# Performance work log

Hardware: AMD Instinct MI355X
Metric: run time of the kernel (lower is better)

## Reference

```python
import jax, jax.numpy as jnp
import numpy as np

B, S, D = 1, 1024, 64
_EPS = 1e-15
_BND = 1.0 - 1e-7  # artanh domain clamp (mirrors geoopt projection)


def _sq(x):
    return jnp.sum(x * x, axis=-1, keepdims=True)


def _nrm(x):
    return jnp.sqrt(_sq(x) + _EPS)


def _normalize(x, axis, eps):
    n = jnp.sqrt(jnp.sum(x * x, axis=axis, keepdims=True))
    return x / jnp.maximum(n, eps)


def _mobius_add(x, y):
    x2, y2 = _sq(x), _sq(y)
    xy = jnp.sum(x * y, axis=-1, keepdims=True)
    num = (1.0 + 2.0 * xy + y2) * x + (1.0 - x2) * y
    den = 1.0 + 2.0 * xy + x2 * y2
    return num / jnp.maximum(den, _EPS)


def _expmap0(u):
    n = _nrm(u)
    return jnp.tanh(n) * u / n


def _logmap0(y):
    n = _nrm(y)
    return jnp.arctanh(jnp.clip(n, 0.0, _BND)) * y / n


def _dist(x, y):
    n = _nrm(_mobius_add(-x, y))[..., 0]
    return 2.0 * jnp.arctanh(jnp.clip(n, 0.0, _BND))


def _logmap(x, y):
    d = _mobius_add(-x, y)
    n = _nrm(d)
    lam = 2.0 / jnp.maximum(1.0 - _sq(x), _EPS)
    return (2.0 / lam) * jnp.arctanh(jnp.clip(n, 0.0, _BND)) * d / n


def _transp0back(x, v):
    return v / jnp.maximum(1.0 - _sq(x), _EPS)


def _forward(q_in, k_in, v_in, Wq, bq, Wk, bk, Wv, bv, Wo, bo,
             tau, gamma, tangent_scale, gumbel_u, v_rand_init):
    q = q_in @ Wq.T + bq
    k = k_in @ Wk.T + bk
    v = v_in @ Wv.T + bv

    q_hyp = _expmap0(q)   # [B,S,D]
    k_hyp = _expmap0(k)

    # all-pairs geodesic distances [B,S,S]
    dist = _dist(q_hyp[:, :, None, :], k_hyp[:, None, :, :])
    min_d = jnp.min(dist, axis=-1, keepdims=True)
    w_un = jnp.exp(-(dist - min_d))                         # unnormalized weights
    w_sum = jnp.sum(w_un, axis=-1, keepdims=True) + 1e-8
    w_probs = w_un / w_sum
    h = jnp.einsum('bqk,bkd->bqd', w_probs, v)

    # Einstein midpoint: weighted Euclidean centroid of pre-map keys -> manifold
    centroid_euc = jnp.einsum('bqk,bkd->bqd', w_un / w_sum, k)
    centroid_hyp = _expmap0(centroid_euc)                   # [B,S,D]

    c2k = _dist(centroid_hyp[:, :, None, :], k_hyp[:, None, :, :])  # [B,S,S]
    wnv = w_un / w_sum
    entropy = -jnp.sum(wnv * jnp.log(wnv + 1e-8), axis=-1, keepdims=True)
    eff_mass = jnp.exp(entropy)
    variance = jnp.sum(wnv * c2k ** 2, axis=-1, keepdims=True)
    tension = variance - tau * eff_mass                     # [B,S,1]

    # matrix-free TPCA power iteration on weighted local tangents
    k_local = _logmap(centroid_hyp[:, :, None, :], k_hyp[:, None, :, :])  # [B,S,S,D]
    weighted_k = k_local * jnp.sqrt(w_un[..., None] + 1e-8)
    v_r = _normalize(v_rand_init, axis=2, eps=1e-12)        # [B,S,D,1]
    for _ in range(3):
        proj = jnp.einsum('bqkd,bqdo->bqko', weighted_k, v_r)
        v_r = jnp.einsum('bqkd,bqko->bqdo', weighted_k, proj)
        v_r = _normalize(v_r, axis=2, eps=1e-12)
    w_proj_local = v_r[..., 0]                              # [B,S,D]
    w_proj_global = _transp0back(centroid_hyp, w_proj_local)

    q_tan = _logmap0(q_hyp)
    c_tan = _logmap0(centroid_hyp)
    fallback = _normalize(q_tan - c_tan, axis=-1, eps=1e-8)
    w_proj = jnp.where(variance > 1e-5, w_proj_global, fallback)

    h_norm = _nrm(h)
    h_comp = jnp.arcsinh(h_norm) * (h / (h_norm + 1e-8))

    # Pitchfork bifurcation (c = 1)
    x = jnp.sum(h_comp * w_proj, axis=-1, keepdims=True)
    diss = (tension > 0).astype(h.dtype)
    h_mag = _nrm(h_comp)
    amplitude = h_mag * jnp.tanh(tension) * diss
    g = -jnp.log(-jnp.log(gumbel_u))                        # gumbel noise, logits = 0
    y_soft = jax.nn.softmax(g / 0.5, axis=-1)
    y_hard = jax.nn.one_hot(jnp.argmax(y_soft, axis=-1), 2, dtype=h.dtype)
    gp = y_soft + jax.lax.stop_gradient(y_hard - y_soft)    # straight-through
    eps_g = (gp[..., 0] - gp[..., 1])[..., None]            # gp @ [1,-1]
    x_star = eps_g * amplitude
    delta_c = jnp.tanh(x_star - x)
    h_prime = h_comp + delta_c * w_proj
    hp_norm = _nrm(h_prime) + 1e-8
    h_pb = h_prime * (jnp.tanh(hp_norm * tangent_scale) / hp_norm)
    h_prime_hyp = _expmap0(h_pb)

    h_out_bif = _logmap0(h_prime_hyp)
    gate = jax.nn.sigmoid(gamma)
    h_fused = (1.0 - gate) * h + gate * h_out_bif
    return h_fused @ Wo.T + bo


def setup_inputs() -> dict:
    key = jax.random.key(0)
    ks = jax.random.split(key, 10)
    std = 0.02
    return {
        'q_in': jax.random.normal(ks[0], (B, S, D), jnp.float32),
        'k_in': jax.random.normal(ks[1], (B, S, D), jnp.float32),
        'v_in': jax.random.normal(ks[2], (B, S, D), jnp.float32),
        'Wq': std * jax.random.normal(ks[3], (D, D), jnp.float32),
        'bq': jnp.zeros((D,), jnp.float32),
        'Wk': std * jax.random.normal(ks[4], (D, D), jnp.float32),
        'bk': jnp.zeros((D,), jnp.float32),
        'Wv': std * jax.random.normal(ks[5], (D, D), jnp.float32),
        'bv': jnp.zeros((D,), jnp.float32),
        'Wo': std * jax.random.normal(ks[6], (D, D), jnp.float32),
        'bo': jnp.zeros((D,), jnp.float32),
        'tau': jnp.float32(5.0),
        'gamma': jnp.float32(0.0),
        'tangent_scale': jnp.float32(0.1),
        'gumbel_u': jax.random.uniform(ks[7], (B, S, 2), jnp.float32, 1e-6, 1.0 - 1e-6),
        'v_rand_init': jax.random.normal(ks[8], (B, S, D, 1), jnp.float32),
    }


def reference(q_in, k_in, v_in, Wq, bq, Wk, bk, Wv, bv, Wo, bo,
              tau, gamma, tangent_scale, gumbel_u, v_rand_init):
    return _forward(q_in, k_in, v_in, Wq, bq, Wk, bk, Wv, bv, Wo, bo,
                    tau, gamma, tangent_scale, gumbel_u, v_rand_init)
```

## Files before the change

### kernel.cpp

```cpp
#include <hip/hip_runtime.h>
#include <math.h>

#define S 1024
#define D 64
#define BND 0.99999994f
#define FINF 3.4e38f
#define C4(v,c) ((&(v).x)[c])

__device__ __forceinline__ float waveSum(float v){
  #pragma unroll
  for(int o=32;o>0;o>>=1) v += __shfl_xor(v,o,64);
  return v;
}
__device__ __forceinline__ float waveMin(float v){
  #pragma unroll
  for(int o=32;o>0;o>>=1) v = fminf(v,__shfl_xor(v,o,64));
  return v;
}
__device__ __forceinline__ float blockSum512(float v, float* red){
  float w = waveSum(v);
  int wid = threadIdx.x>>6;
  __syncthreads();
  if((threadIdx.x&63)==0) red[wid]=w;
  __syncthreads();
  float s=0.f;
  #pragma unroll
  for(int k=0;k<8;k++) s+=red[k];
  return s;
}
__device__ __forceinline__ float blockMin512(float v, float* red){
  float w = waveMin(v);
  int wid = threadIdx.x>>6;
  __syncthreads();
  if((threadIdx.x&63)==0) red[wid]=w;
  __syncthreads();
  float s=red[0];
  #pragma unroll
  for(int k=1;k<8;k++) s=fminf(s,red[k]);
  return s;
}
__device__ __forceinline__ float4 mk4(const float* a){
  float4 r; r.x=a[0]; r.y=a[1]; r.z=a[2]; r.w=a[3]; return r;
}

__global__ __launch_bounds__(64) void k_proj(
  const float* __restrict__ qin, const float* __restrict__ kin, const float* __restrict__ vin,
  const float* __restrict__ Wq, const float* __restrict__ bq,
  const float* __restrict__ Wk, const float* __restrict__ bk,
  const float* __restrict__ Wv, const float* __restrict__ bv,
  const float* __restrict__ vrand,
  float* __restrict__ q_hyp, float* __restrict__ k_hyp, float* __restrict__ kT,
  float* __restrict__ vproj, float* __restrict__ kproj,
  float* __restrict__ q2, float* __restrict__ k2, float* __restrict__ v_r)
{
  const int i = blockIdx.x, d = threadIdx.x;
  __shared__ __align__(16) float lq[D], lk[D], lv[D];
  lq[d]=qin[i*D+d]; lk[d]=kin[i*D+d]; lv[d]=vin[i*D+d];
  __syncthreads();
  float aq=bq[d], ak=bk[d], av=bv[d];
  const float4* wq4=(const float4*)(Wq + d*D);
  const float4* wk4=(const float4*)(Wk + d*D);
  const float4* wv4=(const float4*)(Wv + d*D);
  #pragma unroll
  for(int e=0;e<16;e++){
    float4 a=wq4[e], b=wk4[e], c=wv4[e];
    aq += lq[4*e]*a.x + lq[4*e+1]*a.y + lq[4*e+2]*a.z + lq[4*e+3]*a.w;
    ak += lk[4*e]*b.x + lk[4*e+1]*b.y + lk[4*e+2]*b.z + lk[4*e+3]*b.w;
    av += lv[4*e]*c.x + lv[4*e+1]*c.y + lv[4*e+2]*c.z + lv[4*e+3]*c.w;
  }
  float nq = sqrtf(waveSum(aq*aq)+1e-15f);
  float qh = tanhf(nq)*aq/nq;
  q_hyp[i*D+d]=qh;
  float q2v = waveSum(qh*qh);
  if(d==0) q2[i]=q2v;
  float nk = sqrtf(waveSum(ak*ak)+1e-15f);
  float kh = tanhf(nk)*ak/nk;
  k_hyp[i*D+d]=kh;
  kT[(size_t)d*S + i]=kh;
  float k2v = waveSum(kh*kh);
  if(d==0) k2[i]=k2v;
  vproj[i*D+d]=av;
  kproj[i*D+d]=ak;
  float vr = vrand[i*D+d];
  float nn = sqrtf(waveSum(vr*vr));
  v_r[i*D+d] = vr/fmaxf(nn,1e-12f);
}

__global__ __launch_bounds__(512,4) void k_wc(
  const float* __restrict__ q_hyp, const float* __restrict__ kT,
  const float* __restrict__ q2a, const float* __restrict__ k2a,
  const float* __restrict__ vproj, const float* __restrict__ kproj,
  float* __restrict__ wbuf, float* __restrict__ wsum, float* __restrict__ effm,
  float* __restrict__ h, float* __restrict__ c_hyp, float* __restrict__ c2)
{
  const int i0=blockIdx.x*2, tid=threadIdx.x;
  __shared__ __align__(16) float qv[2][D];
  __shared__ __align__(16) float wl[2][S];
  __shared__ __align__(16) float4 sA[1024];
  __shared__ __align__(16) float4 sB[1024];
  __shared__ float red[8];
  if(tid<128) qv[tid>>6][tid&63]=q_hyp[i0*D+tid];
  __syncthreads();
  const float x20=q2a[i0], x21=q2a[i0+1];
  const float B0=1.f-x20, B1=1.f-x21;
  const int jf=tid&255, dh=tid>>8;
  const float4* kT4=(const float4*)kT;
  {
    float4 p0={0,0,0,0}, p1={0,0,0,0};
    #pragma unroll 8
    for(int dd=0; dd<32; ++dd){
      const int d=(dh<<5)+dd;
      const float4 y=kT4[d*256+jf];
      const float c0=qv[0][d], c1=qv[1][d];
      p0.x+=c0*y.x; p0.y+=c0*y.y; p0.z+=c0*y.z; p0.w+=c0*y.w;
      p1.x+=c1*y.x; p1.y+=c1*y.y; p1.z+=c1*y.z; p1.w+=c1*y.w;
    }
    sA[(dh*2+0)*256+jf]=p0;
    sA[(dh*2+1)*256+jf]=p1;
  }
  __syncthreads();
  float dist[2][4];
  float mn0=FINF, mn1=FINF;
  if(tid<256){
    const float4 qa=sA[jf], qb=sA[512+jf];
    const float4 ra=sA[256+jf], rb=sA[768+jf];
    const float4 y2v=((const float4*)k2a)[jf];
    #pragma unroll
    for(int c=0;c<4;c++){
      const float y2=C4(y2v,c);
      {
        const float dot=C4(qa,c)+C4(qb,c);
        const float A=1.f-2.f*dot+y2;
        const float den=fmaxf(1.f-2.f*dot+x20*y2,1e-15f);
        const float num2=fmaxf(A*A*x20 + B0*B0*y2 - 2.f*A*B0*dot, 0.f);
        const float nn=sqrtf(num2/(den*den)+1e-15f);
        dist[0][c]=2.f*atanhf(fminf(nn,BND));
        mn0=fminf(mn0,dist[0][c]);
      }
      {
        const float dot=C4(ra,c)+C4(rb,c);
        const float A=1.f-2.f*dot+y2;
        const float den=fmaxf(1.f-2.f*dot+x21*y2,1e-15f);
        const float num2=fmaxf(A*A*x21 + B1*B1*y2 - 2.f*A*B1*dot, 0.f);
        const float nn=sqrtf(num2/(den*den)+1e-15f);
        dist[1][c]=2.f*atanhf(fminf(nn,BND));
        mn1=fminf(mn1,dist[1][c]);
      }
    }
  }
  const float m0=blockMin512(mn0,red);
  const float m1=blockMin512(mn1,red);
  float s0=0.f, s1=0.f;
  float w0c[4], w1c[4];
  if(tid<256){
    #pragma unroll
    for(int c=0;c<4;c++){
      w0c[c]=expf(m0-dist[0][c]); s0+=w0c[c];
      w1c[c]=expf(m1-dist[1][c]); s1+=w1c[c];
    }
    ((float4*)&wl[0][0])[jf]=mk4(w0c);
    ((float4*)&wl[1][0])[jf]=mk4(w1c);
    ((float4*)(wbuf+(size_t)i0*S))[jf]=mk4(w0c);
    ((float4*)(wbuf+(size_t)(i0+1)*S))[jf]=mk4(w1c);
  }
  s0=blockSum512(s0,red)+1e-8f;
  s1=blockSum512(s1,red)+1e-8f;
  if(tid==0){ wsum[i0]=s0; wsum[i0+1]=s1; }
  const float inv0=1.f/s0, inv1=1.f/s1;
  float e0=0.f, e1=0.f;
  if(tid<256){
    #pragma unroll
    for(int c=0;c<4;c++){
      const float p0=w0c[c]*inv0; e0 -= p0*logf(p0+1e-8f);
      const float p1=w1c[c]*inv1; e1 -= p1*logf(p1+1e-8f);
    }
  }
  e0=blockSum512(e0,red);
  e1=blockSum512(e1,red);
  if(tid==0){ effm[i0]=expf(e0); effm[i0+1]=expf(e1); }
  const int dq=tid&15, g=tid>>4;
  float4 ah0={0,0,0,0}, ah1={0,0,0,0}, ac0={0,0,0,0}, ac1={0,0,0,0};
  #pragma unroll 4
  for(int jj=0;jj<32;jj++){
    const int j=jj*32+g;
    const float4 yv=((const float4*)(vproj + j*D))[dq];
    const float4 yk=((const float4*)(kproj + j*D))[dq];
    const float u0=wl[0][j], u1=wl[1][j];
    ah0.x+=u0*yv.x; ah0.y+=u0*yv.y; ah0.z+=u0*yv.z; ah0.w+=u0*yv.w;
    ah1.x+=u1*yv.x; ah1.y+=u1*yv.y; ah1.z+=u1*yv.z; ah1.w+=u1*yv.w;
    ac0.x+=u0*yk.x; ac0.y+=u0*yk.y; ac0.z+=u0*yk.z; ac0.w+=u0*yk.w;
    ac1.x+=u1*yk.x; ac1.y+=u1*yk.y; ac1.z+=u1*yk.z; ac1.w+=u1*yk.w;
  }
  float* pA=(float*)sA;
  float* pB=(float*)sB;
  *(float4*)&pA[(g*2+0)*64+dq*4]=ah0;
  *(float4*)&pA[(g*2+1)*64+dq*4]=ah1;
  *(float4*)&pB[(g*2+0)*64+dq*4]=ac0;
  *(float4*)&pB[(g*2+1)*64+dq*4]=ac1;
  __syncthreads();
  if(tid<128){
    const int q=tid>>6, d=tid&63;
    float hs=0.f, cs=0.f;
    #pragma unroll 8
    for(int gg=0;gg<32;gg++){ hs+=pA[(gg*2+q)*64+d]; cs+=pB[(gg*2+q)*64+d]; }
    const float invq = q ? inv1 : inv0;
    h[(i0+q)*D+d]=hs*invq;
    const float ca=cs*invq;
    const float n=sqrtf(waveSum(ca*ca)+1e-15f);
    const float ch=tanhf(n)*ca/n;
    c_hyp[(i0+q)*D+d]=ch;
    const float c2v=waveSum(ch*ch);
    if(d==0) c2[i0+q]=c2v;
  }
}

__global__ __launch_bounds__(512,4) void k_pmega(
  const float* __restrict__ c_hyp, const float* __restrict__ k_hyp,
  const float* __restrict__ kT,
  const float* __restrict__ c2a, const float* __restrict__ k2a,
  const float* __restrict__ wbuf, const float* __restrict__ wsum,
  const float* __restrict__ effm, const float* __restrict__ tau_p,
  const float* __restrict__ h, const float* __restrict__ q_hyp,
  const float* __restrict__ q2a, const float* __restrict__ v_r,
  const float* __restrict__ gu, const float* __restrict__ gamma_p,
  const float* __restrict__ ts_p, const float* __restrict__ Wo,
  const float* __restrict__ bo, float* __restrict__ out)
{
  const int i0=blockIdx.x*2, tid=threadIdx.x;
  __shared__ __align__(16) float cv[2][D];
  __shared__ __align__(16) float vv[2][D];
  __shared__ __align__(16) float aal[2][S];
  __shared__ __align__(16) float bbl[2][S];
  __shared__ __align__(16) float prow[2][S];
  __shared__ __align__(16) float4 sA[1024];
  __shared__ __align__(16) float fus[2][D];
  __shared__ float red[8];
  __shared__ float scal[2][4];

  if(tid<128){ cv[tid>>6][tid&63]=c_hyp[i0*D+tid]; vv[tid>>6][tid&63]=v_r[i0*D+tid]; }
  __syncthreads();
  const float x20=c2a[i0], x21=c2a[i0+1];
  const float Bc0=1.f-x20, Bc1=1.f-x21;
  const float mB0=fmaxf(Bc0,1e-15f), mB1=fmaxf(Bc1,1e-15f);
  const float inv0=1.f/wsum[i0], inv1=1.f/wsum[i0+1];
  const int jf=tid&255, dh=tid>>8;
  const float4* kT4=(const float4*)kT;

  {
    float4 p0={0,0,0,0}, p1={0,0,0,0};
    #pragma unroll 8
    for(int dd=0; dd<32; ++dd){
      const int d=(dh<<5)+dd;
      const float4 y=kT4[d*256+jf];
      const float c0=cv[0][d], c1=cv[1][d];
      p0.x+=c0*y.x; p0.y+=c0*y.y; p0.z+=c0*y.z; p0.w+=c0*y.w;
      p1.x+=c1*y.x; p1.y+=c1*y.y; p1.z+=c1*y.z; p1.w+=c1*y.w;
    }
    sA[(dh*2+0)*256+jf]=p0;
    sA[(dh*2+1)*256+jf]=p1;
  }
  __syncthreads();
  float var0p=0.f, var1p=0.f;
  if(tid<256){
    const float4 qa=sA[jf], qb=sA[512+jf];
    const float4 ra=sA[256+jf], rb=sA[768+jf];
    const float4 y2v=((const float4*)k2a)[jf];
    const float4 w0v=((const float4*)(wbuf+(size_t)i0*S))[jf];
    const float4 w1v=((const float4*)(wbuf+(size_t)(i0+1)*S))[jf];
    float a0c[4],b0c[4],a1c[4],b1c[4];
    #pragma unroll
    for(int c=0;c<4;c++){
      const float y2=C4(y2v,c);
      {
        const float dot=C4(qa,c)+C4(qb,c);
        const float A=1.f-2.f*dot+y2;
        const float den=fmaxf(1.f-2.f*dot+x20*y2,1e-15f);
        const float num2=fmaxf(A*A*x20+Bc0*Bc0*y2-2.f*A*Bc0*dot,0.f);
        const float nn=sqrtf(num2/(den*den)+1e-15f);
        const float art=atanhf(fminf(nn,BND));
        const float w=C4(w0v,c);
        var0p += w*inv0*4.f*art*art;
        const float coef=sqrtf(w+1e-8f)*mB0*art/(nn*den);
        a0c[c]=-coef*A; b0c[c]=coef*Bc0;
      }
      {
        const float dot=C4(ra,c)+C4(rb,c);
        const float A=1.f-2.f*dot+y2;
        const float den=fmaxf(1.f-2.f*dot+x21*y2,1e-15f);
        const float num2=fmaxf(A*A*x21+Bc1*Bc1*y2-2.f*A*Bc1*dot,0.f);
        const float nn=sqrtf(num2/(den*den)+1e-15f);
        const float art=atanhf(fminf(nn,BND));
        const float w=C4(w1v,c);
        var1p += w*inv1*4.f*art*art;
        const float coef=sqrtf(w+1e-8f)*mB1*art/(nn*den);
        a1c[c]=-coef*A; b1c[c]=coef*Bc1;
      }
    }
    ((float4*)&aal[0][0])[jf]=mk4(a0c);
    ((float4*)&aal[1][0])[jf]=mk4(a1c);
    ((float4*)&bbl[0][0])[jf]=mk4(b0c);
    ((float4*)&bbl[1][0])[jf]=mk4(b1c);
  }
  const float var0=blockSum512(var0p,red);
  const float var1=blockSum512(var1p,red);
  if(tid==0){
    scal[0][0]=var0; scal[0][1]=var0 - tau_p[0]*effm[i0];
    scal[1][0]=var1; scal[1][1]=var1 - tau_p[0]*effm[i0+1];
  }

  const int dq=tid&15, g=tid>>4;
  for(int it=0; it<3; ++it){
    __syncthreads();
    if(tid<128){
      const int q=tid>>6, d=tid&63;
      const float cd=waveSum(cv[q][d]*vv[q][d]);
      if(d==0) scal[q][2]=cd;
    }
    __syncthreads();
    const float cdot0=scal[0][2], cdot1=scal[1][2];
    {
      float4 p0={0,0,0,0}, p1={0,0,0,0};
      #pragma unroll 8
      for(int dd=0; dd<32; ++dd){
        const int d=(dh<<5)+dd;
        const float4 y=kT4[d*256+jf];
        const float c0=vv[0][d], c1=vv[1][d];
        p0.x+=c0*y.x; p0.y+=c0*y.y; p0.z+=c0*y.z; p0.w+=c0*y.w;
        p1.x+=c1*y.x; p1.y+=c1*y.y; p1.z+=c1*y.z; p1.w+=c1*y.w;
      }
      sA[(dh*2+0)*256+jf]=p0;
      sA[(dh*2+1)*256+jf]=p1;
    }
    __syncthreads();
    float sal0p=0.f, sal1p=0.f;
    if(tid<256){
      const float4 qa=sA[jf], qb=sA[512+jf];
      const float4 ra=sA[256+jf], rb=sA[768+jf];
      const float4 av0=((float4*)&aal[0][0])[jf];
      const float4 av1=((float4*)&aal[1][0])[jf];
      const float4 bv0=((float4*)&bbl[0][0])[jf];
      const float4 bv1=((float4*)&bbl[1][0])[jf];
      float pr0[4], pr1[4];
      #pragma unroll
      for(int c=0;c<4;c++){
        const float t0=C4(qa,c)+C4(qb,c);
        const float t1=C4(ra,c)+C4(rb,c);
        const float p0=C4(av0,c)*cdot0 + C4(bv0,c)*t0;
        const float p1=C4(av1,c)*cdot1 + C4(bv1,c)*t1;
        pr0[c]=p0*C4(bv0,c); sal0p += p0*C4(av0,c);
        pr1[c]=p1*C4(bv1,c); sal1p += p1*C4(av1,c);
      }
      ((float4*)&prow[0][0])[jf]=mk4(pr0);
      ((float4*)&prow[1][0])[jf]=mk4(pr1);
    }
    const float sal0=blockSum512(sal0p,red);
    const float sal1=blockSum512(sal1p,red);
    float4 a0={0,0,0,0}, a1={0,0,0,0};
    #pragma unroll 4
    for(int jj=0;jj<32;jj++){
      const int j=jj*32+g;
      const float4 y=((const float4*)(k_hyp + j*D))[dq];
      const float u0=prow[0][j], u1=prow[1][j];
      a0.x+=u0*y.x; a0.y+=u0*y.y; a0.z+=u0*y.z; a0.w+=u0*y.w;
      a1.x+=u1*y.x; a1.y+=u1*y.y; a1.z+=u1*y.z; a1.w+=u1*y.w;
    }
    float* pA=(float*)sA;
    *(float4*)&pA[(g*2+0)*64+dq*4]=a0;
    *(float4*)&pA[(g*2+1)*64+dq*4]=a1;
    __syncthreads();
    if(tid<128){
      const int q=tid>>6, d=tid&63;
      float od=(q?sal1:sal0)*cv[q][d];
      #pragma unroll 8
      for(int gg=0;gg<32;gg++) od += pA[(gg*2+q)*64+d];
      const float nn=sqrtf(waveSum(od*od));
      vv[q][d]=od/fmaxf(nn,1e-12f);
    }
  }
  __syncthreads();

  if(tid<128){
    const int q=tid>>6, d=tid&63;
    const int i=i0+q;
    const float x2q = q ? x21 : x20;
    const float vd=vv[q][d];
    const float vars=scal[q][0], tns=scal[q][1];
    const float hd=h[i*D+d];
    const float qd=q_hyp[i*D+d];
    const float q2=q2a[i];
    const float wpg=vd/fmaxf(1.f-x2q,1e-15f);
    const float nq=sqrtf(q2+1e-15f);
    const float qt=atanhf(fminf(nq,BND))*qd/nq;
    const float ncn=sqrtf(x2q+1e-15f);
    const float ct=atanhf(fminf(ncn,BND))*cv[q][d]/ncn;
    const float df=qt-ct;
    const float nd=sqrtf(waveSum(df*df));
    const float fb=df/fmaxf(nd,1e-8f);
    const float wp=(vars>1e-5f)?wpg:fb;
    const float hn=sqrtf(waveSum(hd*hd)+1e-15f);
    const float hc=asinhf(hn)*hd/(hn+1e-8f);
    const float x=waveSum(hc*wp);
    const float hmag=sqrtf(waveSum(hc*hc)+1e-15f);
    const float amp=(tns>0.f)? hmag*tanhf(tns) : 0.f;
    const float u0=gu[i*2], u1=gu[i*2+1];
    const float eg=(u0>=u1)?1.f:-1.f;
    const float dc=tanhf(eg*amp - x);
    const float hp=hc+dc*wp;
    const float hpn=sqrtf(waveSum(hp*hp)+1e-15f)+1e-8f;
    const float hpb=hp*(tanhf(hpn*ts_p[0])/hpn);
    const float n2=sqrtf(waveSum(hpb*hpb)+1e-15f);
    const float hyp=tanhf(n2)*hpb/n2;
    const float n3=sqrtf(waveSum(hyp*hyp)+1e-15f);
    const float bif=atanhf(fminf(n3,BND))*hyp/n3;
    const float gate=1.f/(1.f+expf(-gamma_p[0]));
    fus[q][d]=(1.f-gate)*hd + gate*bif;
  }
  __syncthreads();
  if(tid<128){
    const int q=tid>>6, d=tid&63;
    float acc=bo[d];
    const float4* wo4=(const float4*)(Wo + d*D);
    #pragma unroll
    for(int e=0;e<16;e++){
      float4 wv=wo4[e];
      acc += fus[q][4*e]*wv.x + fus[q][4*e+1]*wv.y + fus[q][4*e+2]*wv.z + fus[q][4*e+3]*wv.w;
    }
    out[(i0+q)*D+d]=acc;
  }
}

extern "C" void kernel_launch(void* const* d_in, const int* in_sizes, int n_in,
                              void* d_out, int out_size, void* d_ws, size_t ws_size,
                              hipStream_t stream)
{
  const float* qin=(const float*)d_in[0];
  const float* kin=(const float*)d_in[1];
  const float* vin=(const float*)d_in[2];
  const float* Wq=(const float*)d_in[3];
  const float* bq=(const float*)d_in[4];
  const float* Wk=(const float*)d_in[5];
  const float* bk=(const float*)d_in[6];
  const float* Wv=(const float*)d_in[7];
  const float* bv=(const float*)d_in[8];
  const float* Wo=(const float*)d_in[9];
  const float* bo=(const float*)d_in[10];
  const float* tau=(const float*)d_in[11];
  const float* gamma=(const float*)d_in[12];
  const float* tscale=(const float*)d_in[13];
  const float* gu=(const float*)d_in[14];
  const float* vrand=(const float*)d_in[15];
  float* out=(float*)d_out;

  float* p=(float*)d_ws;
  float* q_hyp=p; p+=S*D;
  float* k_hyp=p; p+=S*D;
  float* kT=p;    p+=S*D;
  float* vproj=p; p+=S*D;
  float* kproj=p; p+=S*D;
  float* v_r=p;   p+=S*D;
  float* h=p;     p+=S*D;
  float* c_hyp=p; p+=S*D;
  float* q2=p;   p+=S;
  float* k2=p;   p+=S;
  float* c2=p;   p+=S;
  float* wsum=p; p+=S;
  float* effm=p; p+=S;
  float* wbuf=p; p+=(size_t)S*S;

  k_proj<<<S,64,0,stream>>>(qin,kin,vin,Wq,bq,Wk,bk,Wv,bv,vrand,
                            q_hyp,k_hyp,kT,vproj,kproj,q2,k2,v_r);
  k_wc<<<S/2,512,0,stream>>>(q_hyp,kT,q2,k2,vproj,kproj,
                             wbuf,wsum,effm,h,c_hyp,c2);
  k_pmega<<<S/2,512,0,stream>>>(c_hyp,k_hyp,kT,c2,k2,wbuf,wsum,effm,tau,
                                h,q_hyp,q2,v_r,gu,gamma,tscale,Wo,bo,out);
}
```

Baseline: 79.04 us.

## Fuse weight/centroid and power-iteration kernels, process four queries per block

Merges k_wc and k_pmega into a single kernel, so the 1024x1024 weight matrix and the h, c_hyp, wsum and effm intermediates stay in shared memory instead of passing through global memory. Each block now handles four query rows instead of two, which doubles reuse of each kT, vproj, kproj and k_hyp load, and reductions for the four rows are batched into float4 block reductions to save barriers. In exchange there are only 256 blocks, more shared memory per block and a lower occupancy hint, which may underfill the GPU's compute units.

```diff
diff --git a/kernel.cpp b/kernel.cpp
--- a/kernel.cpp
+++ b/kernel.cpp
@@ -12,35 +12,38 @@
   for(int o=32;o>0;o>>=1) v += __shfl_xor(v,o,64);
   return v;
 }
-__device__ __forceinline__ float waveMin(float v){
-  #pragma unroll
-  for(int o=32;o>0;o>>=1) v = fminf(v,__shfl_xor(v,o,64));
-  return v;
-}
-__device__ __forceinline__ float blockSum512(float v, float* red){
-  float w = waveSum(v);
-  int wid = threadIdx.x>>6;
-  __syncthreads();
-  if((threadIdx.x&63)==0) red[wid]=w;
-  __syncthreads();
-  float s=0.f;
-  #pragma unroll
-  for(int k=0;k<8;k++) s+=red[k];
-  return s;
-}
-__device__ __forceinline__ float blockMin512(float v, float* red){
-  float w = waveMin(v);
-  int wid = threadIdx.x>>6;
-  __syncthreads();
-  if((threadIdx.x&63)==0) red[wid]=w;
-  __syncthreads();
-  float s=red[0];
-  #pragma unroll
-  for(int k=1;k<8;k++) s=fminf(s,red[k]);
-  return s;
-}
 __device__ __forceinline__ float4 mk4(const float* a){
   float4 r; r.x=a[0]; r.y=a[1]; r.z=a[2]; r.w=a[3]; return r;
+}
+__device__ __forceinline__ float4 blockSum512_v4(float4 v, float4* red4){
+  #pragma unroll
+  for(int o=32;o>0;o>>=1){
+    v.x+=__shfl_xor(v.x,o,64); v.y+=__shfl_xor(v.y,o,64);
+    v.z+=__shfl_xor(v.z,o,64); v.w+=__shfl_xor(v.w,o,64);
+  }
+  const int wid=threadIdx.x>>6;
+  __syncthreads();
+  if((threadIdx.x&63)==0) red4[wid]=v;
+  __syncthreads();
+  float4 s={0.f,0.f,0.f,0.f};
+  #pragma unroll
+  for(int k=0;k<8;k++){ float4 r=red4[k]; s.x+=r.x; s.y+=r.y; s.z+=r.z; s.w+=r.w; }
+  return s;
+}
+__device__ __forceinline__ float4 blockMin512_v4(float4 v, float4* red4){
+  #pragma unroll
+  for(int o=32;o>0;o>>=1){
+    v.x=fminf(v.x,__shfl_xor(v.x,o,64)); v.y=fminf(v.y,__shfl_xor(v.y,o,64));
+    v.z=fminf(v.z,__shfl_xor(v.z,o,64)); v.w=fminf(v.w,__shfl_xor(v.w,o,64));
+  }
+  const int wid=threadIdx.x>>6;
+  __syncthreads();
+  if((threadIdx.x&63)==0) red4[wid]=v;
+  __syncthreads();
+  float4 s=red4[0];
+  #pragma unroll
+  for(int k=1;k<8;k++){ float4 r=red4[k]; s.x=fminf(s.x,r.x); s.y=fminf(s.y,r.y); s.z=fminf(s.z,r.z); s.w=fminf(s.w,r.w); }
+  return s;
 }
 
 __global__ __launch_bounds__(64) void k_proj(
@@ -86,312 +89,293 @@
   v_r[i*D+d] = vr/fmaxf(nn,1e-12f);
 }
 
-__global__ __launch_bounds__(512,4) void k_wc(
-  const float* __restrict__ q_hyp, const float* __restrict__ kT,
+__global__ __launch_bounds__(512,2) void k_fused(
+  const float* __restrict__ q_hyp_g, const float* __restrict__ k_hyp,
+  const float* __restrict__ kT,
   const float* __restrict__ q2a, const float* __restrict__ k2a,
   const float* __restrict__ vproj, const float* __restrict__ kproj,
-  float* __restrict__ wbuf, float* __restrict__ wsum, float* __restrict__ effm,
-  float* __restrict__ h, float* __restrict__ c_hyp, float* __restrict__ c2)
+  const float* __restrict__ v_r, const float* __restrict__ tau_p,
+  const float* __restrict__ gu, const float* __restrict__ gamma_p,
+  const float* __restrict__ ts_p, const float* __restrict__ Wo,
+  const float* __restrict__ bo, float* __restrict__ out)
 {
-  const int i0=blockIdx.x*2, tid=threadIdx.x;
-  __shared__ __align__(16) float qv[2][D];
-  __shared__ __align__(16) float wl[2][S];
-  __shared__ __align__(16) float4 sA[1024];
-  __shared__ __align__(16) float4 sB[1024];
-  __shared__ float red[8];
-  if(tid<128) qv[tid>>6][tid&63]=q_hyp[i0*D+tid];
-  __syncthreads();
-  const float x20=q2a[i0], x21=q2a[i0+1];
-  const float B0=1.f-x20, B1=1.f-x21;
+  const int i0=blockIdx.x*4, tid=threadIdx.x;
+  __shared__ __align__(16) float qv[4][D];
+  __shared__ __align__(16) float cv[4][D];
+  __shared__ __align__(16) float vv[4][D];
+  __shared__ __align__(16) float hl[4][D];
+  __shared__ __align__(16) float fus[4][D];
+  __shared__ __align__(16) float wl[4][S];
+  __shared__ __align__(16) float aal[4][S];
+  __shared__ __align__(16) float bbl[4][S];
+  __shared__ __align__(16) float4 sA[2048];
+  __shared__ __align__(16) float4 red4[8];
+  __shared__ float scal[4][6];
+  float* const pA=(float*)sA;
+
+  if(tid<256){ qv[tid>>6][tid&63]=q_hyp_g[i0*D+tid]; vv[tid>>6][tid&63]=v_r[i0*D+tid]; }
+  __syncthreads();
+
   const int jf=tid&255, dh=tid>>8;
+  const int qq0=dh, qq1=dh+2;
+  const int dq=tid&15, g=tid>>4;
   const float4* kT4=(const float4*)kT;
+  const float tau=tau_p[0];
+
   {
-    float4 p0={0,0,0,0}, p1={0,0,0,0};
+    float4 p0={0,0,0,0},p1={0,0,0,0},p2={0,0,0,0},p3={0,0,0,0};
     #pragma unroll 8
     for(int dd=0; dd<32; ++dd){
       const int d=(dh<<5)+dd;
       const float4 y=kT4[d*256+jf];
-      const float c0=qv[0][d], c1=qv[1][d];
+      const float c0=qv[0][d], c1=qv[1][d], c2q=qv[2][d], c3=qv[3][d];
       p0.x+=c0*y.x; p0.y+=c0*y.y; p0.z+=c0*y.z; p0.w+=c0*y.w;
       p1.x+=c1*y.x; p1.y+=c1*y.y; p1.z+=c1*y.z; p1.w+=c1*y.w;
-    }
-    sA[(dh*2+0)*256+jf]=p0;
-    sA[(dh*2+1)*256+jf]=p1;
-  }
-  __syncthreads();
-  float dist[2][4];
-  float mn0=FINF, mn1=FINF;
-  if(tid<256){
-    const float4 qa=sA[jf], qb=sA[512+jf];
-    const float4 ra=sA[256+jf], rb=sA[768+jf];
+      p2.x+=c2q*y.x; p2.y+=c2q*y.y; p2.z+=c2q*y.z; p2.w+=c2q*y.w;
+      p3.x+=c3*y.x; p3.y+=c3*y.y; p3.z+=c3*y.z; p3.w+=c3*y.w;
+    }
+    sA[(dh*4+0)*256+jf]=p0; sA[(dh*4+1)*256+jf]=p1;
+    sA[(dh*4+2)*256+jf]=p2; sA[(dh*4+3)*256+jf]=p3;
+  }
+  __syncthreads();
+  float4 inv4;
+  {
     const float4 y2v=((const float4*)k2a)[jf];
+    const float x2q[2]={q2a[i0+qq0], q2a[i0+qq1]};
+    float dist[2][4];
+    float4 mn4={FINF,FINF,FINF,FINF};
     #pragma unroll
-    for(int c=0;c<4;c++){
-      const float y2=C4(y2v,c);
-      {
-        const float dot=C4(qa,c)+C4(qb,c);
+    for(int it=0; it<2; ++it){
+      const int qq = it? qq1:qq0;
+      const float4 da=sA[(0*4+qq)*256+jf], db=sA[(1*4+qq)*256+jf];
+      const float x2=x2q[it], B=1.f-x2;
+      #pragma unroll
+      for(int c=0;c<4;c++){
+        const float y2=C4(y2v,c);
+        const float dot=C4(da,c)+C4(db,c);
         const float A=1.f-2.f*dot+y2;
-        const float den=fmaxf(1.f-2.f*dot+x20*y2,1e-15f);
-        const float num2=fmaxf(A*A*x20 + B0*B0*y2 - 2.f*A*B0*dot, 0.f);
+        const float den=fmaxf(1.f-2.f*dot+x2*y2,1e-15f);
+        const float num2=fmaxf(A*A*x2 + B*B*y2 - 2.f*A*B*dot, 0.f);
         const float nn=sqrtf(num2/(den*den)+1e-15f);
-        dist[0][c]=2.f*atanhf(fminf(nn,BND));
-        mn0=fminf(mn0,dist[0][c]);
-      }
-      {
-        const float dot=C4(ra,c)+C4(rb,c);
-        const float A=1.f-2.f*dot+y2;
-        const float den=fmaxf(1.f-2.f*dot+x21*y2,1e-15f);
-        const float num2=fmaxf(A*A*x21 + B1*B1*y2 - 2.f*A*B1*dot, 0.f);
-        const float nn=sqrtf(num2/(den*den)+1e-15f);
-        dist[1][c]=2.f*atanhf(fminf(nn,BND));
-        mn1=fminf(mn1,dist[1][c]);
-      }
-    }
-  }
-  const float m0=blockMin512(mn0,red);
-  const float m1=blockMin512(mn1,red);
-  float s0=0.f, s1=0.f;
-  float w0c[4], w1c[4];
-  if(tid<256){
+        dist[it][c]=2.f*atanhf(fminf(nn,BND));
+        C4(mn4,qq)=fminf(C4(mn4,qq),dist[it][c]);
+      }
+    }
+    mn4=blockMin512_v4(mn4,red4);
+    float w[2][4];
+    float4 s4={0,0,0,0};
     #pragma unroll
-    for(int c=0;c<4;c++){
-      w0c[c]=expf(m0-dist[0][c]); s0+=w0c[c];
-      w1c[c]=expf(m1-dist[1][c]); s1+=w1c[c];
-    }
-    ((float4*)&wl[0][0])[jf]=mk4(w0c);
-    ((float4*)&wl[1][0])[jf]=mk4(w1c);
-    ((float4*)(wbuf+(size_t)i0*S))[jf]=mk4(w0c);
-    ((float4*)(wbuf+(size_t)(i0+1)*S))[jf]=mk4(w1c);
-  }
-  s0=blockSum512(s0,red)+1e-8f;
-  s1=blockSum512(s1,red)+1e-8f;
-  if(tid==0){ wsum[i0]=s0; wsum[i0+1]=s1; }
-  const float inv0=1.f/s0, inv1=1.f/s1;
-  float e0=0.f, e1=0.f;
-  if(tid<256){
+    for(int it=0; it<2; ++it){
+      const int qq = it? qq1:qq0;
+      #pragma unroll
+      for(int c=0;c<4;c++){ w[it][c]=expf(C4(mn4,qq)-dist[it][c]); C4(s4,qq)+=w[it][c]; }
+      ((float4*)&wl[qq][0])[jf]=mk4(w[it]);
+    }
+    s4=blockSum512_v4(s4,red4);
+    inv4.x=1.f/(s4.x+1e-8f); inv4.y=1.f/(s4.y+1e-8f);
+    inv4.z=1.f/(s4.z+1e-8f); inv4.w=1.f/(s4.w+1e-8f);
+    float4 e4={0,0,0,0};
     #pragma unroll
-    for(int c=0;c<4;c++){
-      const float p0=w0c[c]*inv0; e0 -= p0*logf(p0+1e-8f);
-      const float p1=w1c[c]*inv1; e1 -= p1*logf(p1+1e-8f);
-    }
-  }
-  e0=blockSum512(e0,red);
-  e1=blockSum512(e1,red);
-  if(tid==0){ effm[i0]=expf(e0); effm[i0+1]=expf(e1); }
-  const int dq=tid&15, g=tid>>4;
-  float4 ah0={0,0,0,0}, ah1={0,0,0,0}, ac0={0,0,0,0}, ac1={0,0,0,0};
-  #pragma unroll 4
-  for(int jj=0;jj<32;jj++){
-    const int j=jj*32+g;
-    const float4 yv=((const float4*)(vproj + j*D))[dq];
-    const float4 yk=((const float4*)(kproj + j*D))[dq];
-    const float u0=wl[0][j], u1=wl[1][j];
-    ah0.x+=u0*yv.x; ah0.y+=u0*yv.y; ah0.z+=u0*yv.z; ah0.w+=u0*yv.w;
-    ah1.x+=u1*yv.x; ah1.y+=u1*yv.y; ah1.z+=u1*yv.z; ah1.w+=u1*yv.w;
-    ac0.x+=u0*yk.x; ac0.y+=u0*yk.y; ac0.z+=u0*yk.z; ac0.w+=u0*yk.w;
-    ac1.x+=u1*yk.x; ac1.y+=u1*yk.y; ac1.z+=u1*yk.z; ac1.w+=u1*yk.w;
-  }
-  float* pA=(float*)sA;
-  float* pB=(float*)sB;
-  *(float4*)&pA[(g*2+0)*64+dq*4]=ah0;
-  *(float4*)&pA[(g*2+1)*64+dq*4]=ah1;
-  *(float4*)&pB[(g*2+0)*64+dq*4]=ac0;
-  *(float4*)&pB[(g*2+1)*64+dq*4]=ac1;
-  __syncthreads();
-  if(tid<128){
-    const int q=tid>>6, d=tid&63;
-    float hs=0.f, cs=0.f;
-    #pragma unroll 8
-    for(int gg=0;gg<32;gg++){ hs+=pA[(gg*2+q)*64+d]; cs+=pB[(gg*2+q)*64+d]; }
-    const float invq = q ? inv1 : inv0;
-    h[(i0+q)*D+d]=hs*invq;
-    const float ca=cs*invq;
-    const float n=sqrtf(waveSum(ca*ca)+1e-15f);
-    const float ch=tanhf(n)*ca/n;
-    c_hyp[(i0+q)*D+d]=ch;
-    const float c2v=waveSum(ch*ch);
-    if(d==0) c2[i0+q]=c2v;
-  }
-}
-
-__global__ __launch_bounds__(512,4) void k_pmega(
-  const float* __restrict__ c_hyp, const float* __restrict__ k_hyp,
-  const float* __restrict__ kT,
-  const float* __restrict__ c2a, const float* __restrict__ k2a,
-  const float* __restrict__ wbuf, const float* __restrict__ wsum,
-  const float* __restrict__ effm, const float* __restrict__ tau_p,
-  const float* __restrict__ h, const float* __restrict__ q_hyp,
-  const float* __restrict__ q2a, const float* __restrict__ v_r,
-  const float* __restrict__ gu, const float* __restrict__ gamma_p,
-  const float* __restrict__ ts_p, const float* __restrict__ Wo,
-  const float* __restrict__ bo, float* __restrict__ out)
-{
-  const int i0=blockIdx.x*2, tid=threadIdx.x;
-  __shared__ __align__(16) float cv[2][D];
-  __shared__ __align__(16) float vv[2][D];
-  __shared__ __align__(16) float aal[2][S];
-  __shared__ __align__(16) float bbl[2][S];
-  __shared__ __align__(16) float prow[2][S];
-  __shared__ __align__(16) float4 sA[1024];
-  __shared__ __align__(16) float fus[2][D];
-  __shared__ float red[8];
-  __shared__ float scal[2][4];
-
-  if(tid<128){ cv[tid>>6][tid&63]=c_hyp[i0*D+tid]; vv[tid>>6][tid&63]=v_r[i0*D+tid]; }
-  __syncthreads();
-  const float x20=c2a[i0], x21=c2a[i0+1];
-  const float Bc0=1.f-x20, Bc1=1.f-x21;
-  const float mB0=fmaxf(Bc0,1e-15f), mB1=fmaxf(Bc1,1e-15f);
-  const float inv0=1.f/wsum[i0], inv1=1.f/wsum[i0+1];
-  const int jf=tid&255, dh=tid>>8;
-  const float4* kT4=(const float4*)kT;
+    for(int it=0; it<2; ++it){
+      const int qq = it? qq1:qq0;
+      #pragma unroll
+      for(int c=0;c<4;c++){
+        const float p=w[it][c]*C4(inv4,qq);
+        C4(e4,qq) -= p*logf(p+1e-8f);
+      }
+    }
+    e4=blockSum512_v4(e4,red4);
+    if(tid<4) scal[tid][3]=expf(C4(e4,tid));
+  }
 
   {
-    float4 p0={0,0,0,0}, p1={0,0,0,0};
+    float4 a0={0,0,0,0},a1={0,0,0,0},a2={0,0,0,0},a3={0,0,0,0};
+    #pragma unroll 4
+    for(int jj=0;jj<32;jj++){
+      const int j=jj*32+g;
+      const float4 y=((const float4*)(vproj + j*D))[dq];
+      const float u0=wl[0][j],u1=wl[1][j],u2=wl[2][j],u3=wl[3][j];
+      a0.x+=u0*y.x; a0.y+=u0*y.y; a0.z+=u0*y.z; a0.w+=u0*y.w;
+      a1.x+=u1*y.x; a1.y+=u1*y.y; a1.z+=u1*y.z; a1.w+=u1*y.w;
+      a2.x+=u2*y.x; a2.y+=u2*y.y; a2.z+=u2*y.z; a2.w+=u2*y.w;
+      a3.x+=u3*y.x; a3.y+=u3*y.y; a3.z+=u3*y.z; a3.w+=u3*y.w;
+    }
+    __syncthreads();
+    *(float4*)&pA[(g*4+0)*64+dq*4]=a0; *(float4*)&pA[(g*4+1)*64+dq*4]=a1;
+    *(float4*)&pA[(g*4+2)*64+dq*4]=a2; *(float4*)&pA[(g*4+3)*64+dq*4]=a3;
+    __syncthreads();
+    if(tid<256){
+      const int q=tid>>6, d=tid&63;
+      float hs=0.f;
+      #pragma unroll 8
+      for(int gg=0;gg<32;gg++) hs+=pA[(gg*4+q)*64+d];
+      hl[q][d]=hs*C4(inv4,q);
+    }
+    __syncthreads();
+    float4 b0={0,0,0,0},b1={0,0,0,0},b2={0,0,0,0},b3={0,0,0,0};
+    #pragma unroll 4
+    for(int jj=0;jj<32;jj++){
+      const int j=jj*32+g;
+      const float4 y=((const float4*)(kproj + j*D))[dq];
+      const float u0=wl[0][j],u1=wl[1][j],u2=wl[2][j],u3=wl[3][j];
+      b0.x+=u0*y.x; b0.y+=u0*y.y; b0.z+=u0*y.z; b0.w+=u0*y.w;
+      b1.x+=u1*y.x; b1.y+=u1*y.y; b1.z+=u1*y.z; b1.w+=u1*y.w;
+      b2.x+=u2*y.x; b2.y+=u2*y.y; b2.z+=u2*y.z; b2.w+=u2*y.w;
+      b3.x+=u3*y.x; b3.y+=u3*y.y; b3.z+=u3*y.z; b3.w+=u3*y.w;
+    }
+    *(float4*)&pA[(g*4+0)*64+dq*4]=b0; *(float4*)&pA[(g*4+1)*64+dq*4]=b1;
+    *(float4*)&pA[(g*4+2)*64+dq*4]=b2; *(float4*)&pA[(g*4+3)*64+dq*4]=b3;
+    __syncthreads();
+    if(tid<256){
+      const int q=tid>>6, d=tid&63;
+      float cs=0.f;
+      #pragma unroll 8
+      for(int gg=0;gg<32;gg++) cs+=pA[(gg*4+q)*64+d];
+      const float ca=cs*C4(inv4,q);
+      const float n=sqrtf(waveSum(ca*ca)+1e-15f);
+      const float ch=tanhf(n)*ca/n;
+      cv[q][d]=ch;
+      const float c2v=waveSum(ch*ch);
+      if(d==0) scal[q][4]=c2v;
+    }
+  }
+  __syncthreads();
+
+  {
+    float4 p0={0,0,0,0},p1={0,0,0,0},p2={0,0,0,0},p3={0,0,0,0};
     #pragma unroll 8
     for(int dd=0; dd<32; ++dd){
       const int d=(dh<<5)+dd;
       const float4 y=kT4[d*256+jf];
-      const float c0=cv[0][d], c1=cv[1][d];
+      const float c0=cv[0][d], c1=cv[1][d], c2q=cv[2][d], c3=cv[3][d];
       p0.x+=c0*y.x; p0.y+=c0*y.y; p0.z+=c0*y.z; p0.w+=c0*y.w;
       p1.x+=c1*y.x; p1.y+=c1*y.y; p1.z+=c1*y.z; p1.w+=c1*y.w;
-    }
-    sA[(dh*2+0)*256+jf]=p0;
-    sA[(dh*2+1)*256+jf]=p1;
-  }
-  __syncthreads();
-  float var0p=0.f, var1p=0.f;
-  if(tid<256){
-    const float4 qa=sA[jf], qb=sA[512+jf];
-    const float4 ra=sA[256+jf], rb=sA[768+jf];
+      p2.x+=c2q*y.x; p2.y+=c2q*y.y; p2.z+=c2q*y.z; p2.w+=c2q*y.w;
+      p3.x+=c3*y.x; p3.y+=c3*y.y; p3.z+=c3*y.z; p3.w+=c3*y.w;
+    }
+    sA[(dh*4+0)*256+jf]=p0; sA[(dh*4+1)*256+jf]=p1;
+    sA[(dh*4+2)*256+jf]=p2; sA[(dh*4+3)*256+jf]=p3;
+  }
+  __syncthreads();
+  {
     const float4 y2v=((const float4*)k2a)[jf];
-    const float4 w0v=((const float4*)(wbuf+(size_t)i0*S))[jf];
-    const float4 w1v=((const float4*)(wbuf+(size_t)(i0+1)*S))[jf];
-    float a0c[4],b0c[4],a1c[4],b1c[4];
+    float4 var4={0,0,0,0};
     #pragma unroll
-    for(int c=0;c<4;c++){
-      const float y2=C4(y2v,c);
-      {
-        const float dot=C4(qa,c)+C4(qb,c);
+    for(int it=0; it<2; ++it){
+      const int qq = it? qq1:qq0;
+      const float4 da=sA[(0*4+qq)*256+jf], db=sA[(1*4+qq)*256+jf];
+      const float4 wv=((float4*)&wl[qq][0])[jf];
+      const float x2=scal[qq][4];
+      const float Bc=1.f-x2, mB=fmaxf(Bc,1e-15f), inv=C4(inv4,qq);
+      float ac[4], bc[4];
+      #pragma unroll
+      for(int c=0;c<4;c++){
+        const float y2=C4(y2v,c);
+        const float dot=C4(da,c)+C4(db,c);
         const float A=1.f-2.f*dot+y2;
-        const float den=fmaxf(1.f-2.f*dot+x20*y2,1e-15f);
-        const float num2=fmaxf(A*A*x20+Bc0*Bc0*y2-2.f*A*Bc0*dot,0.f);
+        const float den=fmaxf(1.f-2.f*dot+x2*y2,1e-15f);
+        const float num2=fmaxf(A*A*x2+Bc*Bc*y2-2.f*A*Bc*dot,0.f);
         const float nn=sqrtf(num2/(den*den)+1e-15f);
         const float art=atanhf(fminf(nn,BND));
-        const float w=C4(w0v,c);
-        var0p += w*inv0*4.f*art*art;
-        const float coef=sqrtf(w+1e-8f)*mB0*art/(nn*den);
-        a0c[c]=-coef*A; b0c[c]=coef*Bc0;
-      }
-      {
-        const float dot=C4(ra,c)+C4(rb,c);
-        const float A=1.f-2.f*dot+y2;
-        const float den=fmaxf(1.f-2.f*dot+x21*y2,1e-15f);
-        const float num2=fmaxf(A*A*x21+Bc1*Bc1*y2-2.f*A*Bc1*dot,0.f);
-        const float nn=sqrtf(num2/(den*den)+1e-15f);
-        const float art=atanhf(fminf(nn,BND));
-        const float w=C4(w1v,c);
-        var1p += w*inv1*4.f*art*art;
-        const float coef=sqrtf(w+1e-8f)*mB1*art/(nn*den);
-        a1c[c]=-coef*A; b1c[c]=coef*Bc1;
-      }
-    }
-    ((float4*)&aal[0][0])[jf]=mk4(a0c);
-    ((float4*)&aal[1][0])[jf]=mk4(a1c);
-    ((float4*)&bbl[0][0])[jf]=mk4(b0c);
-    ((float4*)&bbl[1][0])[jf]=mk4(b1c);
-  }
-  const float var0=blockSum512(var0p,red);
-  const float var1=blockSum512(var1p,red);
-  if(tid==0){
-    scal[0][0]=var0; scal[0][1]=var0 - tau_p[0]*effm[i0];
-    scal[1][0]=var1; scal[1][1]=var1 - tau_p[0]*effm[i0+1];
-  }
-
-  const int dq=tid&15, g=tid>>4;
-  for(int it=0; it<3; ++it){
-    __syncthreads();
-    if(tid<128){
+        const float w=C4(wv,c);
+        C4(var4,qq) += w*inv*4.f*art*art;
+        const float coef=sqrtf(w+1e-8f)*mB*art/(nn*den);
+        ac[c]=-coef*A; bc[c]=coef*Bc;
+      }
+      ((float4*)&aal[qq][0])[jf]=mk4(ac);
+      ((float4*)&bbl[qq][0])[jf]=mk4(bc);
+    }
+    var4=blockSum512_v4(var4,red4);
+    if(tid<4){ scal[tid][0]=C4(var4,tid); scal[tid][1]=C4(var4,tid) - tau*scal[tid][3]; }
+  }
+  float* const prow0=&wl[0][0];
+
+  for(int it3=0; it3<3; ++it3){
+    __syncthreads();
+    if(tid<256){
       const int q=tid>>6, d=tid&63;
       const float cd=waveSum(cv[q][d]*vv[q][d]);
       if(d==0) scal[q][2]=cd;
     }
     __syncthreads();
-    const float cdot0=scal[0][2], cdot1=scal[1][2];
+    const float cd0=scal[0][2], cd1=scal[1][2], cd2=scal[2][2], cd3=scal[3][2];
     {
-      float4 p0={0,0,0,0}, p1={0,0,0,0};
+      float4 p0={0,0,0,0},p1={0,0,0,0},p2={0,0,0,0},p3={0,0,0,0};
       #pragma unroll 8
       for(int dd=0; dd<32; ++dd){
         const int d=(dh<<5)+dd;
         const float4 y=kT4[d*256+jf];
-        const float c0=vv[0][d], c1=vv[1][d];
+        const float c0=vv[0][d], c1=vv[1][d], c2q=vv[2][d], c3=vv[3][d];
         p0.x+=c0*y.x; p0.y+=c0*y.y; p0.z+=c0*y.z; p0.w+=c0*y.w;
         p1.x+=c1*y.x; p1.y+=c1*y.y; p1.z+=c1*y.z; p1.w+=c1*y.w;
-      }
-      sA[(dh*2+0)*256+jf]=p0;
-      sA[(dh*2+1)*256+jf]=p1;
-    }
-    __syncthreads();
-    float sal0p=0.f, sal1p=0.f;
+        p2.x+=c2q*y.x; p2.y+=c2q*y.y; p2.z+=c2q*y.z; p2.w+=c2q*y.w;
+        p3.x+=c3*y.x; p3.y+=c3*y.y; p3.z+=c3*y.z; p3.w+=c3*y.w;
+      }
+      sA[(dh*4+0)*256+jf]=p0; sA[(dh*4+1)*256+jf]=p1;
+      sA[(dh*4+2)*256+jf]=p2; sA[(dh*4+3)*256+jf]=p3;
+    }
+    __syncthreads();
+    float4 sal4={0,0,0,0};
+    {
+      const float cdq[2]={ dh? cd1:cd0, dh? cd3:cd2 };
+      #pragma unroll
+      for(int it=0; it<2; ++it){
+        const int qq = it? qq1:qq0;
+        const float4 da=sA[(0*4+qq)*256+jf], db=sA[(1*4+qq)*256+jf];
+        const float4 av=((float4*)&aal[qq][0])[jf];
+        const float4 bv=((float4*)&bbl[qq][0])[jf];
+        float pr[4];
+        #pragma unroll
+        for(int c=0;c<4;c++){
+          const float t=C4(da,c)+C4(db,c);
+          const float p=C4(av,c)*cdq[it] + C4(bv,c)*t;
+          pr[c]=p*C4(bv,c);
+          C4(sal4,qq) += p*C4(av,c);
+        }
+        ((float4*)&prow0[qq*S])[jf]=mk4(pr);
+      }
+    }
+    sal4=blockSum512_v4(sal4,red4);
+    {
+      float4 a0={0,0,0,0},a1={0,0,0,0},a2={0,0,0,0},a3={0,0,0,0};
+      #pragma unroll 4
+      for(int jj=0;jj<32;jj++){
+        const int j=jj*32+g;
+        const float4 y=((const float4*)(k_hyp + j*D))[dq];
+        const float u0=prow0[0*S+j],u1=prow0[1*S+j],u2=prow0[2*S+j],u3=prow0[3*S+j];
+        a0.x+=u0*y.x; a0.y+=u0*y.y; a0.z+=u0*y.z; a0.w+=u0*y.w;
+        a1.x+=u1*y.x; a1.y+=u1*y.y; a1.z+=u1*y.z; a1.w+=u1*y.w;
+        a2.x+=u2*y.x; a2.y+=u2*y.y; a2.z+=u2*y.z; a2.w+=u2*y.w;
+        a3.x+=u3*y.x; a3.y+=u3*y.y; a3.z+=u3*y.z; a3.w+=u3*y.w;
+      }
+      *(float4*)&pA[(g*4+0)*64+dq*4]=a0; *(float4*)&pA[(g*4+1)*64+dq*4]=a1;
+      *(float4*)&pA[(g*4+2)*64+dq*4]=a2; *(float4*)&pA[(g*4+3)*64+dq*4]=a3;
+    }
+    __syncthreads();
     if(tid<256){
-      const float4 qa=sA[jf], qb=sA[512+jf];
-      const float4 ra=sA[256+jf], rb=sA[768+jf];
-      const float4 av0=((float4*)&aal[0][0])[jf];
-      const float4 av1=((float4*)&aal[1][0])[jf];
-      const float4 bv0=((float4*)&bbl[0][0])[jf];
-      const float4 bv1=((float4*)&bbl[1][0])[jf];
-      float pr0[4], pr1[4];
-      #pragma unroll
-      for(int c=0;c<4;c++){
-        const float t0=C4(qa,c)+C4(qb,c);
-        const float t1=C4(ra,c)+C4(rb,c);
-        const float p0=C4(av0,c)*cdot0 + C4(bv0,c)*t0;
-        const float p1=C4(av1,c)*cdot1 + C4(bv1,c)*t1;
-        pr0[c]=p0*C4(bv0,c); sal0p += p0*C4(av0,c);
-        pr1[c]=p1*C4(bv1,c); sal1p += p1*C4(av1,c);
-      }
-      ((float4*)&prow[0][0])[jf]=mk4(pr0);
-      ((float4*)&prow[1][0])[jf]=mk4(pr1);
-    }
-    const float sal0=blockSum512(sal0p,red);
-    const float sal1=blockSum512(sal1p,red);
-    float4 a0={0,0,0,0}, a1={0,0,0,0};
-    #pragma unroll 4
-    for(int jj=0;jj<32;jj++){
-      const int j=jj*32+g;
-      const float4 y=((const float4*)(k_hyp + j*D))[dq];
-      const float u0=prow[0][j], u1=prow[1][j];
-      a0.x+=u0*y.x; a0.y+=u0*y.y; a0.z+=u0*y.z; a0.w+=u0*y.w;
-      a1.x+=u1*y.x; a1.y+=u1*y.y; a1.z+=u1*y.z; a1.w+=u1*y.w;
-    }
-    float* pA=(float*)sA;
-    *(float4*)&pA[(g*2+0)*64+dq*4]=a0;
-    *(float4*)&pA[(g*2+1)*64+dq*4]=a1;
-    __syncthreads();
-    if(tid<128){
       const int q=tid>>6, d=tid&63;
-      float od=(q?sal1:sal0)*cv[q][d];
+      float od=C4(sal4,q)*cv[q][d];
       #pragma unroll 8
-      for(int gg=0;gg<32;gg++) od += pA[(gg*2+q)*64+d];
+      for(int gg=0;gg<32;gg++) od += pA[(gg*4+q)*64+d];
       const float nn=sqrtf(waveSum(od*od));
       vv[q][d]=od/fmaxf(nn,1e-12f);
     }
   }
   __syncthreads();
 
-  if(tid<128){
+  if(tid<256){
     const int q=tid>>6, d=tid&63;
     const int i=i0+q;
-    const float x2q = q ? x21 : x20;
+    const float x2q_c=scal[q][4];
     const float vd=vv[q][d];
     const float vars=scal[q][0], tns=scal[q][1];
-    const float hd=h[i*D+d];
-    const float qd=q_hyp[i*D+d];
+    const float hd=hl[q][d];
+    const float qd=qv[q][d];
     const float q2=q2a[i];
-    const float wpg=vd/fmaxf(1.f-x2q,1e-15f);
+    const float wpg=vd/fmaxf(1.f-x2q_c,1e-15f);
     const float nq=sqrtf(q2+1e-15f);
     const float qt=atanhf(fminf(nq,BND))*qd/nq;
-    const float ncn=sqrtf(x2q+1e-15f);
+    const float ncn=sqrtf(x2q_c+1e-15f);
     const float ct=atanhf(fminf(ncn,BND))*cv[q][d]/ncn;
     const float df=qt-ct;
     const float nd=sqrtf(waveSum(df*df));
@@ -416,7 +400,7 @@
     fus[q][d]=(1.f-gate)*hd + gate*bif;
   }
   __syncthreads();
-  if(tid<128){
+  if(tid<256){
     const int q=tid>>6, d=tid&63;
     float acc=bo[d];
     const float4* wo4=(const float4*)(Wo + d*D);
@@ -458,19 +442,11 @@
   float* vproj=p; p+=S*D;
   float* kproj=p; p+=S*D;
   float* v_r=p;   p+=S*D;
-  float* h=p;     p+=S*D;
-  float* c_hyp=p; p+=S*D;
   float* q2=p;   p+=S;
   float* k2=p;   p+=S;
-  float* c2=p;   p+=S;
-  float* wsum=p; p+=S;
-  float* effm=p; p+=S;
-  float* wbuf=p; p+=(size_t)S*S;
 
   k_proj<<<S,64,0,stream>>>(qin,kin,vin,Wq,bq,Wk,bk,Wv,bv,vrand,
                             q_hyp,k_hyp,kT,vproj,kproj,q2,k2,v_r);
-  k_wc<<<S/2,512,0,stream>>>(q_hyp,kT,q2,k2,vproj,kproj,
-                             wbuf,wsum,effm,h,c_hyp,c2);
-  k_pmega<<<S/2,512,0,stream>>>(c_hyp,k_hyp,kT,c2,k2,wbuf,wsum,effm,tau,
-                                h,q_hyp,q2,v_r,gu,gamma,tscale,Wo,bo,out);
-}
+  k_fused<<<S/4,512,0,stream>>>(q_hyp,k_hyp,kT,q2,k2,vproj,kproj,v_r,
+                                tau,gu,gamma,tscale,Wo,bo,out);
+}
```

Result: slower. 89.96 us (+13.8%).
